# Kernel optimization log

Measured on AMD Instinct MI355X. Metric: run time of the kernel, lower is better.

Reference implementation:

```python
import jax, jax.numpy as jnp
import numpy as np
import math

B, W, D_IN, H = 64, 512, 300, 512

def setup_inputs() -> dict:
    key = jax.random.key(0)
    ks = jax.random.split(key, 8)
    s = 1.0 / math.sqrt(D_IN)
    return {
        "char_vectors": jax.random.normal(ks[0], (B, W, D_IN), jnp.float32),
        "word_vectors": jax.random.normal(ks[1], (B, W, D_IN), jnp.float32),
        "Wk": jax.random.uniform(ks[2], (D_IN, H), jnp.float32, -s, s),
        "bk": jnp.zeros((H,), jnp.float32),
        "Wq": jax.random.uniform(ks[3], (D_IN, H), jnp.float32, -s, s),
        "bq": jnp.zeros((H,), jnp.float32),
        "Wv": jax.random.uniform(ks[4], (D_IN, H), jnp.float32, -s, s),
        "bv": jnp.zeros((H,), jnp.float32),
    }

def reference(char_vectors, word_vectors, Wk, bk, Wq, bq, Wv, bv):
    # Stack word/char reps per word -> [B, W, 2, H]
    def proj(Wm, bm):
        return jnp.stack([word_vectors @ Wm + bm, char_vectors @ Wm + bm], axis=2)
    K = proj(Wk, bk)
    Q = proj(Wq, bq)
    V = proj(Wv, bv)
    temp = jnp.sqrt(jnp.asarray(H, jnp.float32))
    # tiny 2x2 attention per word, fully batched (dropout off = eval mode)
    attn = jnp.einsum("bwqh,bwkh->bwqk", Q, K) / temp
    attn = jax.nn.softmax(attn, axis=-1)
    out = jnp.einsum("bwqk,bwkh->bwqh", attn, V)  # [B, W, 2, H]
    return out.reshape(B, W, 2 * H)
```

## Files before the change

kernel.cpp:

```cpp
#include <hip/hip_runtime.h>

#define D 300
#define KP 328
#define KSTEPS 10
#define ROWS 128
#define WPB 64
#define CH_B 20992
#define BUF_STRIDE 21504
#define NSEG 21

typedef __attribute__((ext_vector_type(4))) float f32x4;
typedef __attribute__((ext_vector_type(8))) short bf16x8;

__device__ inline unsigned short f2bf(float f) {
  unsigned int u = __float_as_uint(f);
  unsigned int r = (u + 0x7fffu + ((u >> 16) & 1u)) >> 16;
  return (unsigned short)r;
}

__device__ inline void gload_lds16(const void* g, void* l) {
  __builtin_amdgcn_global_load_lds(
      (const __attribute__((address_space(1))) unsigned int*)g,
      (__attribute__((address_space(3))) unsigned int*)l, 16, 0, 0);
}

__global__ __launch_bounds__(512) void prep_weights(
    const float* __restrict__ Wq, const float* __restrict__ Wk,
    const float* __restrict__ Wv, unsigned short* __restrict__ wt) {
  int idx = blockIdx.x * 512 + threadIdx.x;
  if (idx >= 1536 * KP) return;
  int n = idx / KP, k = idx - n * KP;
  const float* src = (n < 512) ? Wq : ((n < 1024) ? Wk : Wv);
  int col = n & 511;
  float v = (k < D) ? src[k * 512 + col] : 0.0f;
  wt[idx] = f2bf(v);
}

__global__ __launch_bounds__(512) void fused_attn(
    const float* __restrict__ charv, const float* __restrict__ wordv,
    const unsigned short* __restrict__ wt,
    const float* __restrict__ bk, const float* __restrict__ bq,
    const float* __restrict__ bv, float* __restrict__ out) {
  extern __shared__ char lds[];
  float* biasL = (float*)(lds + 2 * BUF_STRIDE);
  float* sS    = biasL + 1536;
  float* sAt   = sS + 512;

  const int tid  = threadIdx.x;
  const int wid  = tid >> 6;
  const int lane = tid & 63;
  const int lrow = lane & 15;
  const int kgrp = lane >> 4;
  const int rg   = wid >> 1;
  const int cg   = wid & 1;

  auto stage = [&](int t) {
    long base = (t < 32) ? ((long)((t & 1) * 512 + (t >> 1) * 32) * KP * 2)
                         : ((long)(1024 + (t - 32) * 32) * KP * 2);
    const char* srcb = (const char*)wt + base;
    char* dst = lds + (t & 1) * BUF_STRIDE;
    for (int j = wid; j < NSEG; j += 8) {
      int off = j * 1024 + lane * 16;
      const char* src = (off < CH_B) ? (srcb + off) : ((const char*)wt + lane * 16);
      gload_lds16(src, dst + j * 1024);
    }
  };

  stage(0);
  for (int i = tid; i < 1536; i += 512) {
    float v = (i < 512) ? bq[i] : ((i < 1024) ? bk[i - 512] : bv[i - 1024]);
    biasL[i] = v;
  }

  bf16x8 a[2][KSTEPS];
#pragma unroll
  for (int rt = 0; rt < 2; ++rt) {
    int row = blockIdx.x * ROWS + rg * 32 + rt * 16 + lrow;
    const float* rp = ((row & 1) ? charv : wordv) + (row >> 1) * D;
#pragma unroll
    for (int ks = 0; ks < KSTEPS; ++ks) {
      int k0 = ks * 32 + kgrp * 8;
      float4 lo = {0.f, 0.f, 0.f, 0.f}, hi = {0.f, 0.f, 0.f, 0.f};
      if (k0 + 8 <= D) {
        lo = *(const float4*)(rp + k0);
        hi = *(const float4*)(rp + k0 + 4);
      } else if (k0 < D) {
        lo = *(const float4*)(rp + k0);
      }
      bf16x8 v;
      v[0] = (short)f2bf(lo.x); v[1] = (short)f2bf(lo.y);
      v[2] = (short)f2bf(lo.z); v[3] = (short)f2bf(lo.w);
      v[4] = (short)f2bf(hi.x); v[5] = (short)f2bf(hi.y);
      v[6] = (short)f2bf(hi.z); v[7] = (short)f2bf(hi.w);
      a[rt][ks] = v;
    }
  }
  __syncthreads();

  float p[2][8];
#pragma unroll
  for (int rt = 0; rt < 2; ++rt)
#pragma unroll
    for (int t = 0; t < 8; ++t) p[rt][t] = 0.f;

  for (int g = 0; g < 16; ++g) {
    f32x4 accQ[2];
    stage(2 * g + 1);
    {
      float bqv = biasL[g * 32 + cg * 16 + lrow];
#pragma unroll
      for (int rt = 0; rt < 2; ++rt) accQ[rt] = (f32x4){bqv, bqv, bqv, bqv};
      const unsigned short* bp =
          (const unsigned short*)lds + (cg * 16 + lrow) * KP + kgrp * 8;
#pragma unroll
      for (int ks = 0; ks < KSTEPS; ++ks) {
        bf16x8 b = *(const bf16x8*)(bp + ks * 32);
        accQ[0] = __builtin_amdgcn_mfma_f32_16x16x32_bf16(a[0][ks], b, accQ[0], 0, 0, 0);
        accQ[1] = __builtin_amdgcn_mfma_f32_16x16x32_bf16(a[1][ks], b, accQ[1], 0, 0, 0);
      }
    }
    __syncthreads();

    stage(2 * g + 2);
    {
      float bkv = biasL[512 + g * 32 + cg * 16 + lrow];
      f32x4 accK[2];
#pragma unroll
      for (int rt = 0; rt < 2; ++rt) accK[rt] = (f32x4){bkv, bkv, bkv, bkv};
      const unsigned short* bp =
          (const unsigned short*)(lds + BUF_STRIDE) + (cg * 16 + lrow) * KP + kgrp * 8;
#pragma unroll
      for (int ks = 0; ks < KSTEPS; ++ks) {
        bf16x8 b = *(const bf16x8*)(bp + ks * 32);
        accK[0] = __builtin_amdgcn_mfma_f32_16x16x32_bf16(a[0][ks], b, accK[0], 0, 0, 0);
        accK[1] = __builtin_amdgcn_mfma_f32_16x16x32_bf16(a[1][ks], b, accK[1], 0, 0, 0);
      }
#pragma unroll
      for (int rt = 0; rt < 2; ++rt)
#pragma unroll
        for (int wl = 0; wl < 2; ++wl)
#pragma unroll
          for (int i = 0; i < 2; ++i)
#pragma unroll
            for (int j = 0; j < 2; ++j)
              p[rt][wl * 4 + i * 2 + j] += accQ[rt][wl * 2 + i] * accK[rt][wl * 2 + j];
    }
    __syncthreads();
  }

#pragma unroll
  for (int rt = 0; rt < 2; ++rt)
#pragma unroll
    for (int t = 0; t < 8; ++t) {
      float v = p[rt][t];
      v += __shfl_xor(v, 1);
      v += __shfl_xor(v, 2);
      v += __shfl_xor(v, 4);
      v += __shfl_xor(v, 8);
      p[rt][t] = v;
    }
  if (lrow == 0) {
#pragma unroll
    for (int rt = 0; rt < 2; ++rt)
#pragma unroll
      for (int t = 0; t < 8; ++t) {
        int w = rg * 16 + rt * 8 + kgrp * 2 + (t >> 2);
        sS[cg * 256 + w * 4 + (t & 3)] = p[rt][t];
      }
  }
  __syncthreads();
  if (tid < 64) {
    const float sc = 0.044194173824159216f;
    float s[4];
#pragma unroll
    for (int t = 0; t < 4; ++t) s[t] = (sS[tid * 4 + t] + sS[256 + tid * 4 + t]) * sc;
#pragma unroll
    for (int i = 0; i < 2; ++i) {
      float m  = fmaxf(s[i * 2], s[i * 2 + 1]);
      float e0 = expf(s[i * 2] - m), e1 = expf(s[i * 2 + 1] - m);
      float inv = 1.0f / (e0 + e1);
      sAt[tid * 4 + i * 2]     = e0 * inv;
      sAt[tid * 4 + i * 2 + 1] = e1 * inv;
    }
  }
  __syncthreads();

  float at0[2][4], at1[2][4];
#pragma unroll
  for (int rt = 0; rt < 2; ++rt) {
    int wA = rg * 16 + rt * 8 + kgrp * 2;
#pragma unroll
    for (int t = 0; t < 4; ++t) {
      at0[rt][t] = sAt[wA * 4 + t];
      at1[rt][t] = sAt[(wA + 1) * 4 + t];
    }
  }

  for (int t = 32; t < 48; ++t) {
    if (t < 47) stage(t + 1);
    const unsigned short* bufp = (const unsigned short*)(lds + (t & 1) * BUF_STRIDE);
    const int g = t - 32;
    f32x4 accV[2];
    {
      float b = biasL[1024 + g * 32 + cg * 16 + lrow];
      accV[0] = (f32x4){b, b, b, b};
      accV[1] = (f32x4){b, b, b, b};
    }
    const unsigned short* bp = bufp + (cg * 16 + lrow) * KP + kgrp * 8;
#pragma unroll
    for (int ks = 0; ks < KSTEPS; ++ks) {
      bf16x8 b = *(const bf16x8*)(bp + ks * 32);
      accV[0] = __builtin_amdgcn_mfma_f32_16x16x32_bf16(a[0][ks], b, accV[0], 0, 0, 0);
      accV[1] = __builtin_amdgcn_mfma_f32_16x16x32_bf16(a[1][ks], b, accV[1], 0, 0, 0);
    }
#pragma unroll
    for (int rt = 0; rt < 2; ++rt) {
      int gA = blockIdx.x * WPB + rg * 16 + rt * 8 + kgrp * 2;
      int h = g * 32 + cg * 16 + lrow;
      float* o = out + gA * 1024 + h;
      o[0]    = at0[rt][0] * accV[rt][0] + at0[rt][1] * accV[rt][1];
      o[512]  = at0[rt][2] * accV[rt][0] + at0[rt][3] * accV[rt][1];
      o[1024] = at1[rt][0] * accV[rt][2] + at1[rt][1] * accV[rt][3];
      o[1536] = at1[rt][2] * accV[rt][2] + at1[rt][3] * accV[rt][3];
    }
    if (t < 47) __syncthreads();
  }
}

extern "C" void kernel_launch(void* const* d_in, const int* in_sizes, int n_in,
                              void* d_out, int out_size, void* d_ws, size_t ws_size,
                              hipStream_t stream) {
  const float* charv = (const float*)d_in[0];
  const float* wordv = (const float*)d_in[1];
  const float* Wk = (const float*)d_in[2];
  const float* bk = (const float*)d_in[3];
  const float* Wq = (const float*)d_in[4];
  const float* bq = (const float*)d_in[5];
  const float* Wv = (const float*)d_in[6];
  const float* bv = (const float*)d_in[7];
  float* out = (float*)d_out;
  unsigned short* wt = (unsigned short*)d_ws;

  prep_weights<<<(1536 * KP + 511) / 512, 512, 0, stream>>>(Wq, Wk, Wv, wt);

  const int lds_bytes = 2 * BUF_STRIDE + 1536 * 4 + 512 * 4 + 256 * 4;
  fused_attn<<<65536 / ROWS, 512, lds_bytes, stream>>>(charv, wordv, wt, bk, bq, bv, out);
}
```

Before: 102.3 us.

## Read MFMA-fragment-ordered weights directly from global, drop LDS staging and barriers

The bf16 weight layout is changed so each 32-column chunk is stored in MFMA B-fragment order, letting waves load B operands straight from global/L2 instead of staging them through double-buffered LDS with global_load_lds. All per-step __syncthreads, the LDS bias table and dynamic shared memory are removed. The block also shrinks to 256 threads and 64 rows, doubling the grid. Q and K MFMAs are interleaved in one loop. This trades LDS reuse and explicit prefetch for L2 reads and more resident blocks, and adds redundant weight traffic per block.

```diff
diff --git a/kernel.cpp b/kernel.cpp
--- a/kernel.cpp
+++ b/kernel.cpp
@@ -1,13 +1,11 @@
 #include <hip/hip_runtime.h>
 
 #define D 300
-#define KP 328
+#define HDIM 512
+#define ROWS 64
+#define WPB 32
 #define KSTEPS 10
-#define ROWS 128
-#define WPB 64
-#define CH_B 20992
-#define BUF_STRIDE 21504
-#define NSEG 21
+#define CHUNK_ELEMS 10240
 
 typedef __attribute__((ext_vector_type(4))) float f32x4;
 typedef __attribute__((ext_vector_type(8))) short bf16x8;
@@ -18,33 +16,30 @@
   return (unsigned short)r;
 }
 
-__device__ inline void gload_lds16(const void* g, void* l) {
-  __builtin_amdgcn_global_load_lds(
-      (const __attribute__((address_space(1))) unsigned int*)g,
-      (__attribute__((address_space(3))) unsigned int*)l, 16, 0, 0);
-}
-
-__global__ __launch_bounds__(512) void prep_weights(
+__global__ __launch_bounds__(256) void prep_weights(
     const float* __restrict__ Wq, const float* __restrict__ Wk,
     const float* __restrict__ Wv, unsigned short* __restrict__ wt) {
-  int idx = blockIdx.x * 512 + threadIdx.x;
-  if (idx >= 1536 * KP) return;
-  int n = idx / KP, k = idx - n * KP;
-  const float* src = (n < 512) ? Wq : ((n < 1024) ? Wk : Wv);
-  int col = n & 511;
-  float v = (k < D) ? src[k * 512 + col] : 0.0f;
+  int idx = blockIdx.x * 256 + threadIdx.x;
+  if (idx >= 48 * CHUNK_ELEMS) return;
+  int t = idx / CHUNK_ELEMS, r = idx - t * CHUNK_ELEMS;
+  int ks = r >> 10, r2 = r & 1023;
+  int c = r2 >> 5, r3 = r2 & 31;
+  int k = ks * 32 + r3;
+  const float* M;
+  int col0;
+  if (t < 32) { M = (t & 1) ? Wk : Wq; col0 = (t >> 1) * 32; }
+  else        { M = Wv;                col0 = (t - 32) * 32; }
+  float v = (k < D) ? M[k * HDIM + col0 + c] : 0.0f;
   wt[idx] = f2bf(v);
 }
 
-__global__ __launch_bounds__(512) void fused_attn(
+__global__ __launch_bounds__(256) void fused_attn(
     const float* __restrict__ charv, const float* __restrict__ wordv,
     const unsigned short* __restrict__ wt,
     const float* __restrict__ bk, const float* __restrict__ bq,
     const float* __restrict__ bv, float* __restrict__ out) {
-  extern __shared__ char lds[];
-  float* biasL = (float*)(lds + 2 * BUF_STRIDE);
-  float* sS    = biasL + 1536;
-  float* sAt   = sS + 512;
+  __shared__ float sS[256];
+  __shared__ float sAt[128];
 
   const int tid  = threadIdx.x;
   const int wid  = tid >> 6;
@@ -53,24 +48,7 @@
   const int kgrp = lane >> 4;
   const int rg   = wid >> 1;
   const int cg   = wid & 1;
-
-  auto stage = [&](int t) {
-    long base = (t < 32) ? ((long)((t & 1) * 512 + (t >> 1) * 32) * KP * 2)
-                         : ((long)(1024 + (t - 32) * 32) * KP * 2);
-    const char* srcb = (const char*)wt + base;
-    char* dst = lds + (t & 1) * BUF_STRIDE;
-    for (int j = wid; j < NSEG; j += 8) {
-      int off = j * 1024 + lane * 16;
-      const char* src = (off < CH_B) ? (srcb + off) : ((const char*)wt + lane * 16);
-      gload_lds16(src, dst + j * 1024);
-    }
-  };
-
-  stage(0);
-  for (int i = tid; i < 1536; i += 512) {
-    float v = (i < 512) ? bq[i] : ((i < 1024) ? bk[i - 512] : bv[i - 1024]);
-    biasL[i] = v;
-  }
+  const int boff = (cg * 16 + lrow) * 32 + kgrp * 8;
 
   bf16x8 a[2][KSTEPS];
 #pragma unroll
@@ -95,7 +73,6 @@
       a[rt][ks] = v;
     }
   }
-  __syncthreads();
 
   float p[2][8];
 #pragma unroll
@@ -104,48 +81,33 @@
     for (int t = 0; t < 8; ++t) p[rt][t] = 0.f;
 
   for (int g = 0; g < 16; ++g) {
-    f32x4 accQ[2];
-    stage(2 * g + 1);
-    {
-      float bqv = biasL[g * 32 + cg * 16 + lrow];
-#pragma unroll
-      for (int rt = 0; rt < 2; ++rt) accQ[rt] = (f32x4){bqv, bqv, bqv, bqv};
-      const unsigned short* bp =
-          (const unsigned short*)lds + (cg * 16 + lrow) * KP + kgrp * 8;
-#pragma unroll
-      for (int ks = 0; ks < KSTEPS; ++ks) {
-        bf16x8 b = *(const bf16x8*)(bp + ks * 32);
-        accQ[0] = __builtin_amdgcn_mfma_f32_16x16x32_bf16(a[0][ks], b, accQ[0], 0, 0, 0);
-        accQ[1] = __builtin_amdgcn_mfma_f32_16x16x32_bf16(a[1][ks], b, accQ[1], 0, 0, 0);
-      }
-    }
-    __syncthreads();
-
-    stage(2 * g + 2);
-    {
-      float bkv = biasL[512 + g * 32 + cg * 16 + lrow];
-      f32x4 accK[2];
-#pragma unroll
-      for (int rt = 0; rt < 2; ++rt) accK[rt] = (f32x4){bkv, bkv, bkv, bkv};
-      const unsigned short* bp =
-          (const unsigned short*)(lds + BUF_STRIDE) + (cg * 16 + lrow) * KP + kgrp * 8;
-#pragma unroll
-      for (int ks = 0; ks < KSTEPS; ++ks) {
-        bf16x8 b = *(const bf16x8*)(bp + ks * 32);
-        accK[0] = __builtin_amdgcn_mfma_f32_16x16x32_bf16(a[0][ks], b, accK[0], 0, 0, 0);
-        accK[1] = __builtin_amdgcn_mfma_f32_16x16x32_bf16(a[1][ks], b, accK[1], 0, 0, 0);
-      }
-#pragma unroll
-      for (int rt = 0; rt < 2; ++rt)
-#pragma unroll
-        for (int wl = 0; wl < 2; ++wl)
-#pragma unroll
-          for (int i = 0; i < 2; ++i)
-#pragma unroll
-            for (int j = 0; j < 2; ++j)
-              p[rt][wl * 4 + i * 2 + j] += accQ[rt][wl * 2 + i] * accK[rt][wl * 2 + j];
-    }
-    __syncthreads();
+    const bf16x8* cq = (const bf16x8*)(wt + (2 * g) * CHUNK_ELEMS + boff);
+    const bf16x8* ck = (const bf16x8*)(wt + (2 * g + 1) * CHUNK_ELEMS + boff);
+    float bqv = bq[g * 32 + cg * 16 + lrow];
+    float bkv = bk[g * 32 + cg * 16 + lrow];
+    f32x4 accQ[2], accK[2];
+    accQ[0] = (f32x4){bqv, bqv, bqv, bqv};
+    accQ[1] = accQ[0];
+    accK[0] = (f32x4){bkv, bkv, bkv, bkv};
+    accK[1] = accK[0];
+#pragma unroll
+    for (int ks = 0; ks < KSTEPS; ++ks) {
+      bf16x8 bqf = cq[ks * 128];
+      bf16x8 bkf = ck[ks * 128];
+      accQ[0] = __builtin_amdgcn_mfma_f32_16x16x32_bf16(a[0][ks], bqf, accQ[0], 0, 0, 0);
+      accQ[1] = __builtin_amdgcn_mfma_f32_16x16x32_bf16(a[1][ks], bqf, accQ[1], 0, 0, 0);
+      accK[0] = __builtin_amdgcn_mfma_f32_16x16x32_bf16(a[0][ks], bkf, accK[0], 0, 0, 0);
+      accK[1] = __builtin_amdgcn_mfma_f32_16x16x32_bf16(a[1][ks], bkf, accK[1], 0, 0, 0);
+    }
+#pragma unroll
+    for (int rt = 0; rt < 2; ++rt)
+#pragma unroll
+      for (int wl = 0; wl < 2; ++wl)
+#pragma unroll
+        for (int i = 0; i < 2; ++i)
+#pragma unroll
+          for (int j = 0; j < 2; ++j)
+            p[rt][wl * 4 + i * 2 + j] += accQ[rt][wl * 2 + i] * accK[rt][wl * 2 + j];
   }
 
 #pragma unroll
@@ -165,15 +127,15 @@
 #pragma unroll
       for (int t = 0; t < 8; ++t) {
         int w = rg * 16 + rt * 8 + kgrp * 2 + (t >> 2);
-        sS[cg * 256 + w * 4 + (t & 3)] = p[rt][t];
+        sS[cg * 128 + w * 4 + (t & 3)] = p[rt][t];
       }
   }
   __syncthreads();
-  if (tid < 64) {
+  if (tid < 32) {
     const float sc = 0.044194173824159216f;
     float s[4];
 #pragma unroll
-    for (int t = 0; t < 4; ++t) s[t] = (sS[tid * 4 + t] + sS[256 + tid * 4 + t]) * sc;
+    for (int t = 0; t < 4; ++t) s[t] = (sS[tid * 4 + t] + sS[128 + tid * 4 + t]) * sc;
 #pragma unroll
     for (int i = 0; i < 2; ++i) {
       float m  = fmaxf(s[i * 2], s[i * 2 + 1]);
@@ -196,20 +158,15 @@
     }
   }
 
-  for (int t = 32; t < 48; ++t) {
-    if (t < 47) stage(t + 1);
-    const unsigned short* bufp = (const unsigned short*)(lds + (t & 1) * BUF_STRIDE);
-    const int g = t - 32;
+  for (int g = 0; g < 16; ++g) {
+    const bf16x8* cv = (const bf16x8*)(wt + (32 + g) * CHUNK_ELEMS + boff);
+    float bvv = bv[g * 32 + cg * 16 + lrow];
     f32x4 accV[2];
-    {
-      float b = biasL[1024 + g * 32 + cg * 16 + lrow];
-      accV[0] = (f32x4){b, b, b, b};
-      accV[1] = (f32x4){b, b, b, b};
-    }
-    const unsigned short* bp = bufp + (cg * 16 + lrow) * KP + kgrp * 8;
+    accV[0] = (f32x4){bvv, bvv, bvv, bvv};
+    accV[1] = accV[0];
 #pragma unroll
     for (int ks = 0; ks < KSTEPS; ++ks) {
-      bf16x8 b = *(const bf16x8*)(bp + ks * 32);
+      bf16x8 b = cv[ks * 128];
       accV[0] = __builtin_amdgcn_mfma_f32_16x16x32_bf16(a[0][ks], b, accV[0], 0, 0, 0);
       accV[1] = __builtin_amdgcn_mfma_f32_16x16x32_bf16(a[1][ks], b, accV[1], 0, 0, 0);
     }
@@ -223,7 +180,6 @@
       o[1024] = at1[rt][0] * accV[rt][2] + at1[rt][1] * accV[rt][3];
       o[1536] = at1[rt][2] * accV[rt][2] + at1[rt][3] * accV[rt][3];
     }
-    if (t < 47) __syncthreads();
   }
 }
 
@@ -241,8 +197,6 @@
   float* out = (float*)d_out;
   unsigned short* wt = (unsigned short*)d_ws;
 
-  prep_weights<<<(1536 * KP + 511) / 512, 512, 0, stream>>>(Wq, Wk, Wv, wt);
-
-  const int lds_bytes = 2 * BUF_STRIDE + 1536 * 4 + 512 * 4 + 256 * 4;
-  fused_attn<<<65536 / ROWS, 512, lds_bytes, stream>>>(charv, wordv, wt, bk, bq, bv, out);
-}
+  prep_weights<<<(48 * CHUNK_ELEMS + 255) / 256, 256, 0, stream>>>(Wq, Wk, Wv, wt);
+  fused_attn<<<65536 / ROWS, 256, 0, stream>>>(charv, wordv, wt, bk, bq, bv, out);
+}
```

New measurement: 225.0 us. +119.8%, slower.
